# Performance work log

Measured on AMD Instinct MI355X. Metric: run time of the kernel, lower is better.

## Reference

```python
import jax, jax.numpy as jnp
import numpy as np

OUT_IMG = 256
OUT_MSK = 64


def _src_coords(n_out, size):
    # F.interpolate bilinear align_corners=False source coordinates, clamped to edge
    sizef = size.astype(jnp.float32)
    t = (jnp.arange(n_out, dtype=jnp.float32) + 0.5) * (sizef / n_out) - 0.5
    t = jnp.clip(t, 0.0, sizef - 1.0)
    t0 = jnp.floor(t).astype(jnp.int32)
    t1 = jnp.minimum(t0 + 1, size - 1)
    return t0, t1, t - t0.astype(jnp.float32)


def _per_sample(x_img, x_msk, x_bg, pad, sel, color):
    # x_img [3,H,W] float, x_msk [H,W] bool, x_bg [3,Hb,Wb], pad [4] int (l,r,t,b)
    H, W = x_msk.shape
    ys = jnp.any(x_msk, axis=1)
    xs = jnp.any(x_msk, axis=0)
    iy = jnp.arange(H)
    ix = jnp.arange(W)
    miny = jnp.min(jnp.where(ys, iy, H))
    maxy = jnp.max(jnp.where(ys, iy, -1))
    minx = jnp.min(jnp.where(xs, ix, W))
    maxx = jnp.max(jnp.where(xs, ix, -1))
    h = maxy - miny + 1
    w = maxx - minx + 1
    left, right, top, bot = pad[0], pad[1], pad[2], pad[3]
    Hp = h + top + bot   # padded crop height
    Wp = w + left + right  # padded crop width
    # background: real bg image or solid random color (c[ii][-1] > 2 branch)
    bg_sel = jnp.where(sel > 2, x_bg, jnp.broadcast_to(color[:, None, None], x_bg.shape))

    def mask_at(P, Q):
        # value of the padded-cropped mask at integer padded coords (P, Q)
        in_crop = (P >= top) & (P < top + h) & (Q >= left) & (Q < left + w)
        r = jnp.clip(miny + P - top, 0, H - 1)
        c = jnp.clip(minx + Q - left, 0, W - 1)
        return in_crop & x_msk[r, c], r, c

    def sample_img(py, px):
        # composited padded image at integer coords (py x px grid) -> [3,Ho,Wo]
        P = py[:, None]
        Q = px[None, :]
        m, r, c = mask_at(P, Q)
        iv = x_img[:, r, c]
        bv = bg_sel[:, P, Q]
        return jnp.where(m[None], iv, bv)

    def sample_msk(py, px):
        m, _, _ = mask_at(py[:, None], px[None, :])
        return m.astype(jnp.float32)

    def bilinear(sample_fn, n_out, ch_leading):
        y0, y1, wy = _src_coords(n_out, Hp)
        x0, x1, wx = _src_coords(n_out, Wp)
        s00 = sample_fn(y0, x0)
        s01 = sample_fn(y0, x1)
        s10 = sample_fn(y1, x0)
        s11 = sample_fn(y1, x1)
        wy_ = wy[:, None]
        wx_ = wx[None, :]
        if ch_leading:
            wy_ = wy_[None]
            wx_ = wx_[None]
        top_row = s00 * (1.0 - wx_) + s01 * wx_
        bot_row = s10 * (1.0 - wx_) + s11 * wx_
        return top_row * (1.0 - wy_) + bot_row * wy_

    img_out = bilinear(sample_img, OUT_IMG, True)        # [3,256,256]
    msk_out = bilinear(sample_msk, OUT_MSK, False)[None]  # [1,64,64]
    return img_out, msk_out


def _rgb_to_hsv(x):
    r, g, b = x[:, 0], x[:, 1], x[:, 2]
    mx = jnp.max(x, axis=1)
    mn = jnp.min(x, axis=1)
    d = mx - mn
    ds = jnp.where(d > 0, d, 1.0)
    hr = ((g - b) / ds) % 6.0
    hg = (b - r) / ds + 2.0
    hb = (r - g) / ds + 4.0
    hch = jnp.where(mx == r, hr, jnp.where(mx == g, hg, hb)) / 6.0
    hch = jnp.where(d > 0, hch, 0.0)
    s = jnp.where(mx > 0, d / jnp.where(mx > 0, mx, 1.0), 0.0)
    return hch, s, mx


def _hsv_to_rgb(hch, s, v):
    h6 = hch * 6.0
    i = jnp.floor(h6)
    f = h6 - i
    p = v * (1.0 - s)
    q = v * (1.0 - f * s)
    t = v * (1.0 - (1.0 - f) * s)
    im = i.astype(jnp.int32) % 6
    conds = [im == 0, im == 1, im == 2, im == 3, im == 4, im == 5]
    r = jnp.select(conds, [v, q, p, p, t, v])
    g = jnp.select(conds, [t, v, v, q, p, p])
    b = jnp.select(conds, [p, p, t, v, v, q])
    return jnp.stack([r, g, b], axis=1)


def _color_jitter(img, jit):
    # ColorJitter(0.1, 0.1, 0.1, 0.1) with explicit per-sample factors
    b = (0.9 + 0.2 * jit[:, 0])[:, None, None, None]
    c = (0.9 + 0.2 * jit[:, 1])[:, None, None, None]
    s = (0.9 + 0.2 * jit[:, 2])[:, None, None, None]
    hd = (-0.1 + 0.2 * jit[:, 3])[:, None, None]
    img = jnp.clip(img * b, 0.0, 1.0)
    gray = (0.299 * img[:, 0] + 0.587 * img[:, 1] + 0.114 * img[:, 2])[:, None]
    mean = jnp.mean(gray, axis=(2, 3), keepdims=True)
    img = jnp.clip(c * img + (1.0 - c) * mean, 0.0, 1.0)
    gray = (0.299 * img[:, 0] + 0.587 * img[:, 1] + 0.114 * img[:, 2])[:, None]
    img = jnp.clip(s * img + (1.0 - s) * gray, 0.0, 1.0)
    hch, sa, v = _rgb_to_hsv(img)
    hch = (hch + hd) % 1.0
    return jnp.clip(_hsv_to_rgb(hch, sa, v), 0.0, 1.0)


def setup_inputs() -> dict:
    key = jax.random.key(0)
    ks = jax.random.split(key, 7)
    B, H, W = 64, 448, 448
    return {
        "img": jax.random.uniform(ks[0], (B, 3, H, W), jnp.float32),
        "ms": jax.random.uniform(ks[1], (B, 1, H, W), jnp.float32),
        "bg": jax.random.uniform(ks[2], (B, 3, H + 40, W + 40), jnp.float32),
        "pads": jax.random.randint(ks[3], (B, 4), 0, 20, jnp.int32),
        "csel": jax.random.randint(ks[4], (B,), 0, 20, jnp.int32),
        "rand_color": jax.random.uniform(ks[5], (B, 3), jnp.float32),
        "jitter": jax.random.uniform(ks[6], (B, 4), jnp.float32),
    }


def reference(img, ms, bg, pads, csel, rand_color, jitter):
    mask = ms[:, 0] > 0.5
    img_out, msk_out = jax.vmap(_per_sample)(img, mask, bg, pads, csel, rand_color)
    img_out = _color_jitter(img_out, jitter)
    return img_out, msk_out
```

## Files before the change

kernel.cpp:

```cpp
#include <hip/hip_runtime.h>

#define H_IN 448
#define W_IN 448
#define HW_IN (H_IN * W_IN)
#define BGW 488
#define BGHW (BGW * BGW)
#define OUTI 256
#define OUTI_PIX (OUTI * OUTI)
#define OUTM 64
#define B_SAMPLES 64
#define BBOX_CHUNKS 16
#define BBOX_ROWS (H_IN / BBOX_CHUNKS)
#define BITS_STRIDE 8

typedef unsigned long long u64;

__device__ __forceinline__ float clamp01(float x) { return fminf(fmaxf(x, 0.f), 1.f); }
__device__ __forceinline__ int clampi(int x, int lo, int hi) { return min(max(x, lo), hi); }

__global__ void k_bbox(const float* __restrict__ ms, int* __restrict__ bbox,
                       u64* __restrict__ bits) {
    int b = blockIdx.y, chunk = blockIdx.x;
    int tid = threadIdx.x;
    int wave = tid >> 6, lane = tid & 63;
    const float* msB = ms + (size_t)b * HW_IN;
    u64* bitsB = bits + (size_t)b * H_IN * BITS_STRIDE;

    int miny = H_IN, maxy = -1, minx = W_IN, maxx = -1;
    for (int rr = wave; rr < BBOX_ROWS; rr += 4) {
        int row = chunk * BBOX_ROWS + rr;
        const float4* rowp = (const float4*)(msB + (size_t)row * W_IN);
#pragma unroll
        for (int sub = 0; sub < 2; ++sub) {
            int c4 = sub * 64 + lane;
            bool valid = c4 < (W_IN / 4);
            float4 v = rowp[min(c4, W_IN / 4 - 1)];
            bool a0 = valid && (v.x > 0.5f);
            bool a1 = valid && (v.y > 0.5f);
            bool a2 = valid && (v.z > 0.5f);
            bool a3 = valid && (v.w > 0.5f);
            u64 b0 = __ballot(a0), b1 = __ballot(a1), b2 = __ballot(a2), b3 = __ballot(a3);
            if (a0 | a1 | a2 | a3) {
                miny = min(miny, row); maxy = max(maxy, row);
                int xb = c4 * 4;
                if (a0) { minx = min(minx, xb);     maxx = max(maxx, xb); }
                if (a1) { minx = min(minx, xb + 1); maxx = max(maxx, xb + 1); }
                if (a2) { minx = min(minx, xb + 2); maxx = max(maxx, xb + 2); }
                if (a3) { minx = min(minx, xb + 3); maxx = max(maxx, xb + 3); }
            }
            if (lane < 4) {
                u64 w = (lane == 0) ? b0 : (lane == 1) ? b1 : (lane == 2) ? b2 : b3;
                bitsB[(size_t)row * BITS_STRIDE + sub * 4 + lane] = w;
            }
        }
    }
    __shared__ int s[4];
    if (tid == 0) { s[0] = H_IN; s[1] = -1; s[2] = W_IN; s[3] = -1; }
    __syncthreads();
    atomicMin(&s[0], miny); atomicMax(&s[1], maxy);
    atomicMin(&s[2], minx); atomicMax(&s[3], maxx);
    __syncthreads();
    if (tid == 0) {
        atomicMin(&bbox[b * 4 + 0], s[0]);
        atomicMin(&bbox[b * 4 + 1], -s[1]);
        atomicMin(&bbox[b * 4 + 2], s[2]);
        atomicMin(&bbox[b * 4 + 3], -s[3]);
    }
}

struct Geo {
    int miny, minx, h, w, top, left, Hp, Wp;
};
__device__ __forceinline__ Geo load_geo(const int* __restrict__ bbox,
                                        const int* __restrict__ pads, int b) {
    Geo g;
    g.miny = bbox[b * 4 + 0];
    int maxy = -bbox[b * 4 + 1];
    g.minx = bbox[b * 4 + 2];
    int maxx = -bbox[b * 4 + 3];
    int left = pads[b * 4 + 0], right = pads[b * 4 + 1];
    int top = pads[b * 4 + 2], bot = pads[b * 4 + 3];
    g.h = maxy - g.miny + 1;
    g.w = maxx - g.minx + 1;
    g.top = top; g.left = left;
    g.Hp = g.h + top + bot;
    g.Wp = g.w + left + right;
    return g;
}

__device__ __forceinline__ void src_coord(int i, int n_out, int size,
                                          int& t0, int& t1, float& frac) {
    float sizef = (float)size;
    float t = (i + 0.5f) * (sizef / (float)n_out) - 0.5f;
    t = fminf(fmaxf(t, 0.f), sizef - 1.f);
    t0 = (int)floorf(t);
    t1 = min(t0 + 1, size - 1);
    frac = t - (float)t0;
}

__device__ __forceinline__ bool mask_bit(const u64* rowbits, int c) {
    u64 w = rowbits[((c >> 8) << 2) | (c & 3)];
    return (w >> ((c >> 2) & 63)) & 1ULL;
}

__global__ void __launch_bounds__(256) k_resize_img(
        const float* __restrict__ img, const float* __restrict__ bg,
        const int* __restrict__ pads, const int* __restrict__ csel,
        const float* __restrict__ rcol, const float* __restrict__ jit,
        const int* __restrict__ bbox, const u64* __restrict__ bits,
        unsigned short* __restrict__ mid, float* __restrict__ partials) {
    int oy = blockIdx.x;
    int b = blockIdx.y;
    int tid = threadIdx.x;

    Geo g = load_geo(bbox, pads, b);
    bool useBg = csel[b] > 2;
    float c0 = rcol[b * 3 + 0], c1 = rcol[b * 3 + 1], c2 = rcol[b * 3 + 2];
    float bfac = 0.9f + 0.2f * jit[b * 4 + 0];

    int y0, y1; float wy;
    src_coord(oy, OUTI, g.Hp, y0, y1, wy);
    int r0 = clampi(g.miny + y0 - g.top, 0, H_IN - 1);
    int r1 = clampi(g.miny + y1 - g.top, 0, H_IN - 1);
    bool incy0 = (y0 >= g.top) && (y0 < g.top + g.h);
    bool incy1 = (y1 >= g.top) && (y1 < g.top + g.h);

    __shared__ float s_im[6][W_IN];
    __shared__ float s_bg[6][BGW];
    __shared__ u64 s_bits[2][BITS_STRIDE];

    const float* imB = img + (size_t)b * 3 * HW_IN;
    const u64* bitsB = bits + (size_t)b * H_IN * BITS_STRIDE;

#pragma unroll
    for (int k = 0; k < 3; ++k) {
        int item = k * 256 + tid;
        int p = item >> 7;
        int idx = item & 127;
        if (idx < W_IN / 4) {
            int ky = p > 2;
            int ch = p - 3 * ky;
            int row = ky ? r1 : r0;
            ((float4*)s_im[p])[idx] =
                ((const float4*)(imB + (size_t)ch * HW_IN + (size_t)row * W_IN))[idx];
        }
    }
    if (useBg) {
        const float* bgB = bg + (size_t)b * 3 * BGHW;
#pragma unroll
        for (int k = 0; k < 3; ++k) {
            int item = k * 256 + tid;
            int p = item >> 7;
            int idx = item & 127;
            if (idx < BGW / 4) {
                int ky = p > 2;
                int ch = p - 3 * ky;
                int row = ky ? y1 : y0;
                ((float4*)s_bg[p])[idx] =
                    ((const float4*)(bgB + (size_t)ch * BGHW + (size_t)row * BGW))[idx];
            }
        }
    }
    if (tid < 16) {
        int ky = tid >> 3, idx = tid & 7;
        s_bits[ky][idx] = bitsB[(size_t)(ky ? r1 : r0) * BITS_STRIDE + idx];
    }
    __syncthreads();

    int x0, x1; float wx;
    src_coord(tid, OUTI, g.Wp, x0, x1, wx);

    float acc0 = 0.f, acc1 = 0.f, acc2 = 0.f;
#pragma unroll
    for (int tap = 0; tap < 4; ++tap) {
        int ky = tap >> 1;
        int ky3 = ky * 3;
        int Q = (tap & 1) ? x1 : x0;
        float wgt = (ky ? wy : 1.f - wy) * ((tap & 1) ? wx : 1.f - wx);
        bool incy = ky ? incy1 : incy0;
        bool in_crop = incy && (Q >= g.left) && (Q < g.left + g.w);
        int c = clampi(g.minx + Q - g.left, 0, W_IN - 1);
        bool mm = in_crop && mask_bit(s_bits[ky], c);
        float i0 = s_im[ky3 + 0][c], i1 = s_im[ky3 + 1][c], i2 = s_im[ky3 + 2][c];
        float b0, b1, b2;
        if (useBg) {
            b0 = s_bg[ky3 + 0][Q]; b1 = s_bg[ky3 + 1][Q]; b2 = s_bg[ky3 + 2][Q];
        } else {
            b0 = c0; b1 = c1; b2 = c2;
        }
        acc0 += wgt * (mm ? i0 : b0);
        acc1 += wgt * (mm ? i1 : b1);
        acc2 += wgt * (mm ? i2 : b2);
    }
    float o0 = clamp01(acc0 * bfac);
    float o1 = clamp01(acc1 * bfac);
    float o2 = clamp01(acc2 * bfac);
    size_t o = (size_t)b * 3 * OUTI_PIX + (size_t)oy * OUTI + tid;
    mid[o] = (unsigned short)__float2uint_rn(o0 * 65535.f);
    mid[o + OUTI_PIX] = (unsigned short)__float2uint_rn(o1 * 65535.f);
    mid[o + 2 * OUTI_PIX] = (unsigned short)__float2uint_rn(o2 * 65535.f);

    float gsum = 0.299f * o0 + 0.587f * o1 + 0.114f * o2;
#pragma unroll
    for (int off = 32; off > 0; off >>= 1) gsum += __shfl_down(gsum, off, 64);
    __shared__ float ls[4];
    int wid = tid >> 6, lane = tid & 63;
    if (lane == 0) ls[wid] = gsum;
    __syncthreads();
    if (tid == 0)
        partials[b * 256 + oy] = ls[0] + ls[1] + ls[2] + ls[3];
}

__global__ void k_resize_msk(const u64* __restrict__ bits, const int* __restrict__ pads,
                             const int* __restrict__ bbox, float* __restrict__ outm) {
    int b = blockIdx.y;
    int pix = blockIdx.x * blockDim.x + threadIdx.x;
    int oy = pix >> 6, ox = pix & 63;

    Geo g = load_geo(bbox, pads, b);
    int y0, y1, x0, x1; float wy, wx;
    src_coord(oy, OUTM, g.Hp, y0, y1, wy);
    src_coord(ox, OUTM, g.Wp, x0, x1, wx);

    const u64* bitsB = bits + (size_t)b * H_IN * BITS_STRIDE;
    float acc = 0.f;
#pragma unroll
    for (int tap = 0; tap < 4; ++tap) {
        int P = (tap & 2) ? y1 : y0;
        int Q = (tap & 1) ? x1 : x0;
        float wgt = ((tap & 2) ? wy : 1.f - wy) * ((tap & 1) ? wx : 1.f - wx);
        bool in_crop = (P >= g.top) && (P < g.top + g.h) && (Q >= g.left) && (Q < g.left + g.w);
        int r = clampi(g.miny + P - g.top, 0, H_IN - 1);
        int c = clampi(g.minx + Q - g.left, 0, W_IN - 1);
        bool mm = in_crop && mask_bit(bitsB + (size_t)r * BITS_STRIDE, c);
        acc += wgt * (mm ? 1.f : 0.f);
    }
    outm[(size_t)b * (OUTM * OUTM) + pix] = acc;
}

__device__ __forceinline__ void jitter_px(float& r, float& g, float& bl,
                                          float cc, float ssf, float hd, float mean) {
    r = clamp01(cc * r + (1.f - cc) * mean);
    g = clamp01(cc * g + (1.f - cc) * mean);
    bl = clamp01(cc * bl + (1.f - cc) * mean);
    float gray = 0.299f * r + 0.587f * g + 0.114f * bl;
    r = clamp01(ssf * r + (1.f - ssf) * gray);
    g = clamp01(ssf * g + (1.f - ssf) * gray);
    bl = clamp01(ssf * bl + (1.f - ssf) * gray);
    float mx = fmaxf(r, fmaxf(g, bl));
    float mn = fminf(r, fminf(g, bl));
    float d = mx - mn;
    float dsv = (d > 0.f) ? d : 1.f;
    float hch;
    if (mx == r) {
        float t = (g - bl) / dsv;
        t = fmodf(t, 6.f);
        if (t < 0.f) t += 6.f;
        hch = t;
    } else if (mx == g) {
        hch = (bl - r) / dsv + 2.f;
    } else {
        hch = (r - g) / dsv + 4.f;
    }
    hch = (d > 0.f) ? hch * (1.f / 6.f) : 0.f;
    float sat = (mx > 0.f) ? d / mx : 0.f;
    float v = mx;
    float hh = hch + hd;
    hh -= floorf(hh);
    float h6 = hh * 6.f;
    float fi = floorf(h6);
    float f = h6 - fi;
    float pp = v * (1.f - sat);
    float q = v * (1.f - f * sat);
    float t = v * (1.f - (1.f - f) * sat);
    int im = ((int)fi) % 6;
    float ro, go, bo;
    switch (im) {
        case 0: ro = v;  go = t;  bo = pp; break;
        case 1: ro = q;  go = v;  bo = pp; break;
        case 2: ro = pp; go = v;  bo = t;  break;
        case 3: ro = pp; go = q;  bo = v;  break;
        case 4: ro = t;  go = pp; bo = v;  break;
        default: ro = v; go = pp; bo = q;  break;
    }
    r = clamp01(ro); g = clamp01(go); bl = clamp01(bo);
}

__global__ void k_jitter(const unsigned short* __restrict__ mid,
                         float* __restrict__ out, const float* __restrict__ jit,
                         const float* __restrict__ partials) {
    int b = blockIdx.y;
    int tid = threadIdx.x;

    float pv = partials[b * 256 + tid];
#pragma unroll
    for (int off = 32; off > 0; off >>= 1) pv += __shfl_down(pv, off, 64);
    __shared__ float ls[4];
    int wid = tid >> 6, lane = tid & 63;
    if (lane == 0) ls[wid] = pv;
    __syncthreads();
    float mean = (ls[0] + ls[1] + ls[2] + ls[3]) * (1.f / (float)OUTI_PIX);

    float cc = 0.9f + 0.2f * jit[b * 4 + 1];
    float ssf = 0.9f + 0.2f * jit[b * 4 + 2];
    float hd = -0.1f + 0.2f * jit[b * 4 + 3];

    int idx4 = blockIdx.x * blockDim.x + tid;
    const ushort4* mr = (const ushort4*)(mid + (size_t)b * 3 * OUTI_PIX) + idx4;
    const ushort4* mg = mr + OUTI_PIX / 4;
    const ushort4* mb = mr + 2 * (OUTI_PIX / 4);
    ushort4 ur = *mr, ug = *mg, ub = *mb;

    const float S = 1.f / 65535.f;
    float r0 = ur.x * S, r1 = ur.y * S, r2 = ur.z * S, r3 = ur.w * S;
    float g0 = ug.x * S, g1 = ug.y * S, g2 = ug.z * S, g3 = ug.w * S;
    float b0 = ub.x * S, b1 = ub.y * S, b2 = ub.z * S, b3 = ub.w * S;

    jitter_px(r0, g0, b0, cc, ssf, hd, mean);
    jitter_px(r1, g1, b1, cc, ssf, hd, mean);
    jitter_px(r2, g2, b2, cc, ssf, hd, mean);
    jitter_px(r3, g3, b3, cc, ssf, hd, mean);

    float4* pr = (float4*)(out + (size_t)b * 3 * OUTI_PIX) + idx4;
    float4* pg = pr + OUTI_PIX / 4;
    float4* pb = pr + 2 * (OUTI_PIX / 4);
    *pr = make_float4(r0, r1, r2, r3);
    *pg = make_float4(g0, g1, g2, g3);
    *pb = make_float4(b0, b1, b2, b3);
}

extern "C" void kernel_launch(void* const* d_in, const int* in_sizes, int n_in,
                              void* d_out, int out_size, void* d_ws, size_t ws_size,
                              hipStream_t stream) {
    const float* img = (const float*)d_in[0];
    const float* ms = (const float*)d_in[1];
    const float* bg = (const float*)d_in[2];
    const int* pads = (const int*)d_in[3];
    const int* csel = (const int*)d_in[4];
    const float* rcol = (const float*)d_in[5];
    const float* jit = (const float*)d_in[6];
    float* out = (float*)d_out;

    int* bbox = (int*)d_ws;
    float* partials = (float*)((char*)d_ws + 1024);
    u64* bits = (u64*)((char*)d_ws + 1024 + 65536);
    unsigned short* mid = (unsigned short*)((char*)d_ws + (2u << 20));
    float* outm = out + (size_t)B_SAMPLES * 3 * OUTI_PIX;

    hipMemsetAsync(bbox, 0x7F, B_SAMPLES * 4 * sizeof(int), stream);

    k_bbox<<<dim3(BBOX_CHUNKS, B_SAMPLES), 256, 0, stream>>>(ms, bbox, bits);
    k_resize_img<<<dim3(OUTI, B_SAMPLES), 256, 0, stream>>>(
        img, bg, pads, csel, rcol, jit, bbox, bits, mid, partials);
    k_resize_msk<<<dim3((OUTM * OUTM) / 256, B_SAMPLES), 256, 0, stream>>>(
        bits, pads, bbox, outm);
    k_jitter<<<dim3(OUTI_PIX / 4 / 256, B_SAMPLES), 256, 0, stream>>>(
        mid, out, jit, partials);
}
```

Before: 123.3 us.

## Process four output rows per block, sharing a u16-quantized source row span

Each resize block now computes four consecutive output rows. It loads the contiguous span of image and background source rows once into shared memory, stored as 16-bit values. This cuts the repeated global loads of overlapping source rows and quarters the block count, with the per-row gray partial sums folded into one value per group. The cost is that inputs are quantized to 16 bits before interpolation, which adds a small precision loss, and the shared-memory span is fixed at ten rows.

```diff
diff --git a/kernel.cpp b/kernel.cpp
--- a/kernel.cpp
+++ b/kernel.cpp
@@ -12,6 +12,9 @@
 #define BBOX_CHUNKS 16
 #define BBOX_ROWS (H_IN / BBOX_CHUNKS)
 #define BITS_STRIDE 8
+#define RPB 4
+#define NGRP (OUTI / RPB)
+#define SPAN 10
 
 typedef unsigned long long u64;
 
@@ -103,13 +106,32 @@
     return (w >> ((c >> 2) & 63)) & 1ULL;
 }
 
+struct RowGeom {
+    int y0, y1, r0, r1;
+    float wy;
+    bool incy0, incy1;
+};
+__device__ __forceinline__ RowGeom row_geom(const Geo& g, int oy) {
+    RowGeom rg;
+    src_coord(oy, OUTI, g.Hp, rg.y0, rg.y1, rg.wy);
+    rg.r0 = clampi(g.miny + rg.y0 - g.top, 0, H_IN - 1);
+    rg.r1 = clampi(g.miny + rg.y1 - g.top, 0, H_IN - 1);
+    rg.incy0 = (rg.y0 >= g.top) && (rg.y0 < g.top + g.h);
+    rg.incy1 = (rg.y1 >= g.top) && (rg.y1 < g.top + g.h);
+    return rg;
+}
+
+__device__ __forceinline__ unsigned short q16(float x) {
+    return (unsigned short)__float2uint_rn(x * 65535.f);
+}
+
 __global__ void __launch_bounds__(256) k_resize_img(
         const float* __restrict__ img, const float* __restrict__ bg,
         const int* __restrict__ pads, const int* __restrict__ csel,
         const float* __restrict__ rcol, const float* __restrict__ jit,
         const int* __restrict__ bbox, const u64* __restrict__ bits,
         unsigned short* __restrict__ mid, float* __restrict__ partials) {
-    int oy = blockIdx.x;
+    int grp = blockIdx.x;
     int b = blockIdx.y;
     int tid = threadIdx.x;
 
@@ -118,97 +140,110 @@
     float c0 = rcol[b * 3 + 0], c1 = rcol[b * 3 + 1], c2 = rcol[b * 3 + 2];
     float bfac = 0.9f + 0.2f * jit[b * 4 + 0];
 
-    int y0, y1; float wy;
-    src_coord(oy, OUTI, g.Hp, y0, y1, wy);
-    int r0 = clampi(g.miny + y0 - g.top, 0, H_IN - 1);
-    int r1 = clampi(g.miny + y1 - g.top, 0, H_IN - 1);
-    bool incy0 = (y0 >= g.top) && (y0 < g.top + g.h);
-    bool incy1 = (y1 >= g.top) && (y1 < g.top + g.h);
-
-    __shared__ float s_im[6][W_IN];
-    __shared__ float s_bg[6][BGW];
-    __shared__ u64 s_bits[2][BITS_STRIDE];
+    RowGeom rg[RPB];
+#pragma unroll
+    for (int t = 0; t < RPB; ++t) rg[t] = row_geom(g, grp * RPB + t);
+    int R0 = rg[0].r0, R1 = rg[RPB - 1].r1;
+    int Y0 = rg[0].y0, Y1 = rg[RPB - 1].y1;
+    int NRi = R1 - R0 + 1;
+    int NRb = Y1 - Y0 + 1;
+
+    __shared__ unsigned short s_im[3][SPAN][W_IN];
+    __shared__ unsigned short s_bg[3][SPAN][BGW];
+    __shared__ u64 s_bits[SPAN][BITS_STRIDE];
+    __shared__ float ls[4];
 
     const float* imB = img + (size_t)b * 3 * HW_IN;
     const u64* bitsB = bits + (size_t)b * H_IN * BITS_STRIDE;
 
 #pragma unroll
-    for (int k = 0; k < 3; ++k) {
-        int item = k * 256 + tid;
-        int p = item >> 7;
-        int idx = item & 127;
-        if (idx < W_IN / 4) {
-            int ky = p > 2;
-            int ch = p - 3 * ky;
-            int row = ky ? r1 : r0;
-            ((float4*)s_im[p])[idx] =
-                ((const float4*)(imB + (size_t)ch * HW_IN + (size_t)row * W_IN))[idx];
+    for (int ch = 0; ch < 3; ++ch) {
+        const float4* src = (const float4*)(imB + (size_t)ch * HW_IN + (size_t)R0 * W_IN);
+        int n4 = NRi * (W_IN / 4);
+        for (int i = tid; i < n4; i += 256) {
+            int row = i / (W_IN / 4);
+            int idx = i - row * (W_IN / 4);
+            float4 v = src[i];
+            ushort4 u = {q16(v.x), q16(v.y), q16(v.z), q16(v.w)};
+            *(ushort4*)&s_im[ch][row][idx * 4] = u;
         }
     }
     if (useBg) {
         const float* bgB = bg + (size_t)b * 3 * BGHW;
 #pragma unroll
-        for (int k = 0; k < 3; ++k) {
-            int item = k * 256 + tid;
-            int p = item >> 7;
-            int idx = item & 127;
-            if (idx < BGW / 4) {
-                int ky = p > 2;
-                int ch = p - 3 * ky;
-                int row = ky ? y1 : y0;
-                ((float4*)s_bg[p])[idx] =
-                    ((const float4*)(bgB + (size_t)ch * BGHW + (size_t)row * BGW))[idx];
+        for (int ch = 0; ch < 3; ++ch) {
+            const float4* src = (const float4*)(bgB + (size_t)ch * BGHW + (size_t)Y0 * BGW);
+            int n4 = NRb * (BGW / 4);
+            for (int i = tid; i < n4; i += 256) {
+                int row = i / (BGW / 4);
+                int idx = i - row * (BGW / 4);
+                float4 v = src[i];
+                ushort4 u = {q16(v.x), q16(v.y), q16(v.z), q16(v.w)};
+                *(ushort4*)&s_bg[ch][row][idx * 4] = u;
             }
         }
     }
-    if (tid < 16) {
-        int ky = tid >> 3, idx = tid & 7;
-        s_bits[ky][idx] = bitsB[(size_t)(ky ? r1 : r0) * BITS_STRIDE + idx];
+    if (tid < NRi * BITS_STRIDE) {
+        int row = tid >> 3, idx = tid & 7;
+        s_bits[row][idx] = bitsB[(size_t)(R0 + row) * BITS_STRIDE + idx];
     }
     __syncthreads();
 
     int x0, x1; float wx;
     src_coord(tid, OUTI, g.Wp, x0, x1, wx);
-
-    float acc0 = 0.f, acc1 = 0.f, acc2 = 0.f;
-#pragma unroll
-    for (int tap = 0; tap < 4; ++tap) {
-        int ky = tap >> 1;
-        int ky3 = ky * 3;
-        int Q = (tap & 1) ? x1 : x0;
-        float wgt = (ky ? wy : 1.f - wy) * ((tap & 1) ? wx : 1.f - wx);
-        bool incy = ky ? incy1 : incy0;
-        bool in_crop = incy && (Q >= g.left) && (Q < g.left + g.w);
-        int c = clampi(g.minx + Q - g.left, 0, W_IN - 1);
-        bool mm = in_crop && mask_bit(s_bits[ky], c);
-        float i0 = s_im[ky3 + 0][c], i1 = s_im[ky3 + 1][c], i2 = s_im[ky3 + 2][c];
-        float b0, b1, b2;
-        if (useBg) {
-            b0 = s_bg[ky3 + 0][Q]; b1 = s_bg[ky3 + 1][Q]; b2 = s_bg[ky3 + 2][Q];
-        } else {
-            b0 = c0; b1 = c1; b2 = c2;
+    int cA = clampi(g.minx + x0 - g.left, 0, W_IN - 1);
+    int cB = clampi(g.minx + x1 - g.left, 0, W_IN - 1);
+    bool inxA = (x0 >= g.left) && (x0 < g.left + g.w);
+    bool inxB = (x1 >= g.left) && (x1 < g.left + g.w);
+
+    const float S = 1.f / 65535.f;
+    float gacc = 0.f;
+#pragma unroll
+    for (int t = 0; t < RPB; ++t) {
+        float acc0 = 0.f, acc1 = 0.f, acc2 = 0.f;
+#pragma unroll
+        for (int tap = 0; tap < 4; ++tap) {
+            int ky = tap >> 1;
+            int Q = (tap & 1) ? x1 : x0;
+            int c = (tap & 1) ? cB : cA;
+            float wgt = (ky ? rg[t].wy : 1.f - rg[t].wy) * ((tap & 1) ? wx : 1.f - wx);
+            bool incy = ky ? rg[t].incy1 : rg[t].incy0;
+            bool in_crop = incy && ((tap & 1) ? inxB : inxA);
+            int rr = (ky ? rg[t].r1 : rg[t].r0) - R0;
+            bool mm = in_crop && mask_bit(s_bits[rr], c);
+            float i0 = s_im[0][rr][c] * S;
+            float i1 = s_im[1][rr][c] * S;
+            float i2 = s_im[2][rr][c] * S;
+            float b0, b1, b2;
+            if (useBg) {
+                int br = (ky ? rg[t].y1 : rg[t].y0) - Y0;
+                b0 = s_bg[0][br][Q] * S;
+                b1 = s_bg[1][br][Q] * S;
+                b2 = s_bg[2][br][Q] * S;
+            } else {
+                b0 = c0; b1 = c1; b2 = c2;
+            }
+            acc0 += wgt * (mm ? i0 : b0);
+            acc1 += wgt * (mm ? i1 : b1);
+            acc2 += wgt * (mm ? i2 : b2);
         }
-        acc0 += wgt * (mm ? i0 : b0);
-        acc1 += wgt * (mm ? i1 : b1);
-        acc2 += wgt * (mm ? i2 : b2);
-    }
-    float o0 = clamp01(acc0 * bfac);
-    float o1 = clamp01(acc1 * bfac);
-    float o2 = clamp01(acc2 * bfac);
-    size_t o = (size_t)b * 3 * OUTI_PIX + (size_t)oy * OUTI + tid;
-    mid[o] = (unsigned short)__float2uint_rn(o0 * 65535.f);
-    mid[o + OUTI_PIX] = (unsigned short)__float2uint_rn(o1 * 65535.f);
-    mid[o + 2 * OUTI_PIX] = (unsigned short)__float2uint_rn(o2 * 65535.f);
-
-    float gsum = 0.299f * o0 + 0.587f * o1 + 0.114f * o2;
-#pragma unroll
-    for (int off = 32; off > 0; off >>= 1) gsum += __shfl_down(gsum, off, 64);
-    __shared__ float ls[4];
-    int wid = tid >> 6, lane = tid & 63;
-    if (lane == 0) ls[wid] = gsum;
+        float o0 = clamp01(acc0 * bfac);
+        float o1 = clamp01(acc1 * bfac);
+        float o2 = clamp01(acc2 * bfac);
+        size_t o = (size_t)b * 3 * OUTI_PIX + (size_t)(grp * RPB + t) * OUTI + tid;
+        mid[o] = q16(o0);
+        mid[o + OUTI_PIX] = q16(o1);
+        mid[o + 2 * OUTI_PIX] = q16(o2);
+        gacc += 0.299f * o0 + 0.587f * o1 + 0.114f * o2;
+    }
+
+#pragma unroll
+    for (int off = 32; off > 0; off >>= 1) gacc += __shfl_down(gacc, off, 64);
+    int wave = tid >> 6, lane = tid & 63;
+    if (lane == 0) ls[wave] = gacc;
     __syncthreads();
     if (tid == 0)
-        partials[b * 256 + oy] = ls[0] + ls[1] + ls[2] + ls[3];
+        partials[b * NGRP + grp] = ls[0] + ls[1] + ls[2] + ls[3];
 }
 
 __global__ void k_resize_msk(const u64* __restrict__ bits, const int* __restrict__ pads,
@@ -292,7 +327,7 @@
     int b = blockIdx.y;
     int tid = threadIdx.x;
 
-    float pv = partials[b * 256 + tid];
+    float pv = (tid < NGRP) ? partials[b * NGRP + tid] : 0.f;
 #pragma unroll
     for (int off = 32; off > 0; off >>= 1) pv += __shfl_down(pv, off, 64);
     __shared__ float ls[4];
@@ -350,7 +385,7 @@
     hipMemsetAsync(bbox, 0x7F, B_SAMPLES * 4 * sizeof(int), stream);
 
     k_bbox<<<dim3(BBOX_CHUNKS, B_SAMPLES), 256, 0, stream>>>(ms, bbox, bits);
-    k_resize_img<<<dim3(OUTI, B_SAMPLES), 256, 0, stream>>>(
+    k_resize_img<<<dim3(NGRP, B_SAMPLES), 256, 0, stream>>>(
         img, bg, pads, csel, rcol, jit, bbox, bits, mid, partials);
     k_resize_msk<<<dim3((OUTM * OUTM) / 256, B_SAMPLES), 256, 0, stream>>>(
         bits, pads, bbox, outm);
```

Measured after the change: 200.1 us. 62.3% more time.

## Split image resize rows into half-width blocks loading only a 256-column window

Applied to the files above, without the earlier changes.

Each output row of the image resize is now handled by two 128-thread blocks, each staging only a 256-column window of the source image and background rows into shared memory instead of the full rows. The point is to cut global loads and shared-memory footprint per block and to launch more, smaller blocks. Per-block brightness partials double and the jitter kernel sums both halves. The bbox kernel also gets twice as many chunks. The window assumes the source span of 128 output columns fits in 256 columns, which holds only when the padded crop width is at most about 512.

```diff
diff --git a/kernel.cpp b/kernel.cpp
--- a/kernel.cpp
+++ b/kernel.cpp
@@ -9,9 +9,10 @@
 #define OUTI_PIX (OUTI * OUTI)
 #define OUTM 64
 #define B_SAMPLES 64
-#define BBOX_CHUNKS 16
+#define BBOX_CHUNKS 32
 #define BBOX_ROWS (H_IN / BBOX_CHUNKS)
 #define BITS_STRIDE 8
+#define WIN 256
 
 typedef unsigned long long u64;
 
@@ -103,15 +104,22 @@
     return (w >> ((c >> 2) & 63)) & 1ULL;
 }
 
-__global__ void __launch_bounds__(256) k_resize_img(
+__device__ __forceinline__ unsigned short q16(float x) {
+    return (unsigned short)__float2uint_rn(x * 65535.f);
+}
+
+__global__ void __launch_bounds__(128) k_resize_img(
         const float* __restrict__ img, const float* __restrict__ bg,
         const int* __restrict__ pads, const int* __restrict__ csel,
         const float* __restrict__ rcol, const float* __restrict__ jit,
         const int* __restrict__ bbox, const u64* __restrict__ bits,
         unsigned short* __restrict__ mid, float* __restrict__ partials) {
-    int oy = blockIdx.x;
+    int bx = blockIdx.x;
+    int oy = bx >> 1;
+    int h = bx & 1;
     int b = blockIdx.y;
     int tid = threadIdx.x;
+    int col = h * 128 + tid;
 
     Geo g = load_geo(bbox, pads, b);
     bool useBg = csel[b] > 2;
@@ -125,40 +133,43 @@
     bool incy0 = (y0 >= g.top) && (y0 < g.top + g.h);
     bool incy1 = (y1 >= g.top) && (y1 < g.top + g.h);
 
-    __shared__ float s_im[6][W_IN];
-    __shared__ float s_bg[6][BGW];
+    int xw0, xw1d; float wdum;
+    src_coord(h * 128, OUTI, g.Wp, xw0, xw1d, wdum);
+    int cW = clampi(g.minx + xw0 - g.left, 0, W_IN - 1);
+    int cStart = min(cW & ~3, W_IN - WIN);
+    int qStart = min(xw0 & ~3, BGW - WIN);
+
+    __shared__ float s_im[6][WIN];
+    __shared__ float s_bg[6][WIN];
     __shared__ u64 s_bits[2][BITS_STRIDE];
+    __shared__ float ls[2];
 
     const float* imB = img + (size_t)b * 3 * HW_IN;
     const u64* bitsB = bits + (size_t)b * H_IN * BITS_STRIDE;
 
 #pragma unroll
     for (int k = 0; k < 3; ++k) {
-        int item = k * 256 + tid;
-        int p = item >> 7;
-        int idx = item & 127;
-        if (idx < W_IN / 4) {
+        int item = k * 128 + tid;
+        int p = item >> 6;
+        int idx = item & 63;
+        int ky = p > 2;
+        int ch = p - 3 * ky;
+        int row = ky ? r1 : r0;
+        ((float4*)s_im[p])[idx] =
+            ((const float4*)(imB + (size_t)ch * HW_IN + (size_t)row * W_IN + cStart))[idx];
+    }
+    if (useBg) {
+        const float* bgB = bg + (size_t)b * 3 * BGHW;
+#pragma unroll
+        for (int k = 0; k < 3; ++k) {
+            int item = k * 128 + tid;
+            int p = item >> 6;
+            int idx = item & 63;
             int ky = p > 2;
             int ch = p - 3 * ky;
-            int row = ky ? r1 : r0;
-            ((float4*)s_im[p])[idx] =
-                ((const float4*)(imB + (size_t)ch * HW_IN + (size_t)row * W_IN))[idx];
-        }
-    }
-    if (useBg) {
-        const float* bgB = bg + (size_t)b * 3 * BGHW;
-#pragma unroll
-        for (int k = 0; k < 3; ++k) {
-            int item = k * 256 + tid;
-            int p = item >> 7;
-            int idx = item & 127;
-            if (idx < BGW / 4) {
-                int ky = p > 2;
-                int ch = p - 3 * ky;
-                int row = ky ? y1 : y0;
-                ((float4*)s_bg[p])[idx] =
-                    ((const float4*)(bgB + (size_t)ch * BGHW + (size_t)row * BGW))[idx];
-            }
+            int row = ky ? y1 : y0;
+            ((float4*)s_bg[p])[idx] =
+                ((const float4*)(bgB + (size_t)ch * BGHW + (size_t)row * BGW + qStart))[idx];
         }
     }
     if (tid < 16) {
@@ -168,7 +179,7 @@
     __syncthreads();
 
     int x0, x1; float wx;
-    src_coord(tid, OUTI, g.Wp, x0, x1, wx);
+    src_coord(col, OUTI, g.Wp, x0, x1, wx);
 
     float acc0 = 0.f, acc1 = 0.f, acc2 = 0.f;
 #pragma unroll
@@ -181,10 +192,12 @@
         bool in_crop = incy && (Q >= g.left) && (Q < g.left + g.w);
         int c = clampi(g.minx + Q - g.left, 0, W_IN - 1);
         bool mm = in_crop && mask_bit(s_bits[ky], c);
-        float i0 = s_im[ky3 + 0][c], i1 = s_im[ky3 + 1][c], i2 = s_im[ky3 + 2][c];
+        int cl = c - cStart;
+        float i0 = s_im[ky3 + 0][cl], i1 = s_im[ky3 + 1][cl], i2 = s_im[ky3 + 2][cl];
         float b0, b1, b2;
         if (useBg) {
-            b0 = s_bg[ky3 + 0][Q]; b1 = s_bg[ky3 + 1][Q]; b2 = s_bg[ky3 + 2][Q];
+            int ql = Q - qStart;
+            b0 = s_bg[ky3 + 0][ql]; b1 = s_bg[ky3 + 1][ql]; b2 = s_bg[ky3 + 2][ql];
         } else {
             b0 = c0; b1 = c1; b2 = c2;
         }
@@ -195,20 +208,19 @@
     float o0 = clamp01(acc0 * bfac);
     float o1 = clamp01(acc1 * bfac);
     float o2 = clamp01(acc2 * bfac);
-    size_t o = (size_t)b * 3 * OUTI_PIX + (size_t)oy * OUTI + tid;
-    mid[o] = (unsigned short)__float2uint_rn(o0 * 65535.f);
-    mid[o + OUTI_PIX] = (unsigned short)__float2uint_rn(o1 * 65535.f);
-    mid[o + 2 * OUTI_PIX] = (unsigned short)__float2uint_rn(o2 * 65535.f);
+    size_t o = (size_t)b * 3 * OUTI_PIX + (size_t)oy * OUTI + col;
+    mid[o] = q16(o0);
+    mid[o + OUTI_PIX] = q16(o1);
+    mid[o + 2 * OUTI_PIX] = q16(o2);
 
     float gsum = 0.299f * o0 + 0.587f * o1 + 0.114f * o2;
 #pragma unroll
     for (int off = 32; off > 0; off >>= 1) gsum += __shfl_down(gsum, off, 64);
-    __shared__ float ls[4];
-    int wid = tid >> 6, lane = tid & 63;
-    if (lane == 0) ls[wid] = gsum;
+    int wave = tid >> 6, lane = tid & 63;
+    if (lane == 0) ls[wave] = gsum;
     __syncthreads();
     if (tid == 0)
-        partials[b * 256 + oy] = ls[0] + ls[1] + ls[2] + ls[3];
+        partials[b * 512 + bx] = ls[0] + ls[1];
 }
 
 __global__ void k_resize_msk(const u64* __restrict__ bits, const int* __restrict__ pads,
@@ -292,7 +304,7 @@
     int b = blockIdx.y;
     int tid = threadIdx.x;
 
-    float pv = partials[b * 256 + tid];
+    float pv = partials[b * 512 + tid] + partials[b * 512 + 256 + tid];
 #pragma unroll
     for (int off = 32; off > 0; off >>= 1) pv += __shfl_down(pv, off, 64);
     __shared__ float ls[4];
@@ -343,14 +355,14 @@
 
     int* bbox = (int*)d_ws;
     float* partials = (float*)((char*)d_ws + 1024);
-    u64* bits = (u64*)((char*)d_ws + 1024 + 65536);
+    u64* bits = (u64*)((char*)d_ws + 1024 + 512 * B_SAMPLES * 4);
     unsigned short* mid = (unsigned short*)((char*)d_ws + (2u << 20));
     float* outm = out + (size_t)B_SAMPLES * 3 * OUTI_PIX;
 
     hipMemsetAsync(bbox, 0x7F, B_SAMPLES * 4 * sizeof(int), stream);
 
     k_bbox<<<dim3(BBOX_CHUNKS, B_SAMPLES), 256, 0, stream>>>(ms, bbox, bits);
-    k_resize_img<<<dim3(OUTI, B_SAMPLES), 256, 0, stream>>>(
+    k_resize_img<<<dim3(OUTI * 2, B_SAMPLES), 128, 0, stream>>>(
         img, bg, pads, csel, rcol, jit, bbox, bits, mid, partials);
     k_resize_msk<<<dim3((OUTM * OUTM) / 256, B_SAMPLES), 256, 0, stream>>>(
         bits, pads, bbox, outm);
```

After: 137.2 us. +11.3%, slower.

## Process two output rows per block and stage source rows in LDS as 16-bit

Applied to the files above, without the earlier changes.

The image resize kernel now handles two output rows per 512-thread block instead of one row per 256-thread block, loading four source rows per block. The staged image and background rows are quantized to 16-bit unsigned in shared memory to halve LDS footprint and allow higher occupancy. Partial sums are reduced per row pair, and the jitter kernel is adjusted to read 128 partials. Adjacent output rows often share source rows, yet each row's pair is still loaded separately, so little global traffic is saved. The extra quantization adds conversion work and slight precision loss.

```diff
diff --git a/kernel.cpp b/kernel.cpp
--- a/kernel.cpp
+++ b/kernel.cpp
@@ -17,6 +17,9 @@
 
 __device__ __forceinline__ float clamp01(float x) { return fminf(fmaxf(x, 0.f), 1.f); }
 __device__ __forceinline__ int clampi(int x, int lo, int hi) { return min(max(x, lo), hi); }
+__device__ __forceinline__ unsigned short q16(float x) {
+    return (unsigned short)__float2uint_rn(x * 65535.f);
+}
 
 __global__ void k_bbox(const float* __restrict__ ms, int* __restrict__ bbox,
                        u64* __restrict__ bits) {
@@ -103,88 +106,114 @@
     return (w >> ((c >> 2) & 63)) & 1ULL;
 }
 
-__global__ void __launch_bounds__(256) k_resize_img(
+struct RowGeom {
+    int y0, y1, r0, r1;
+    float wy;
+    bool incy0, incy1;
+};
+__device__ __forceinline__ RowGeom row_geom(const Geo& g, int oy) {
+    RowGeom rg;
+    src_coord(oy, OUTI, g.Hp, rg.y0, rg.y1, rg.wy);
+    rg.r0 = clampi(g.miny + rg.y0 - g.top, 0, H_IN - 1);
+    rg.r1 = clampi(g.miny + rg.y1 - g.top, 0, H_IN - 1);
+    rg.incy0 = (rg.y0 >= g.top) && (rg.y0 < g.top + g.h);
+    rg.incy1 = (rg.y1 >= g.top) && (rg.y1 < g.top + g.h);
+    return rg;
+}
+
+__global__ void __launch_bounds__(512, 8) k_resize_img(
         const float* __restrict__ img, const float* __restrict__ bg,
         const int* __restrict__ pads, const int* __restrict__ csel,
         const float* __restrict__ rcol, const float* __restrict__ jit,
         const int* __restrict__ bbox, const u64* __restrict__ bits,
         unsigned short* __restrict__ mid, float* __restrict__ partials) {
-    int oy = blockIdx.x;
+    int pair = blockIdx.x;
     int b = blockIdx.y;
     int tid = threadIdx.x;
+    int trow = tid >> 8;
+    int col = tid & 255;
 
     Geo g = load_geo(bbox, pads, b);
     bool useBg = csel[b] > 2;
     float c0 = rcol[b * 3 + 0], c1 = rcol[b * 3 + 1], c2 = rcol[b * 3 + 2];
     float bfac = 0.9f + 0.2f * jit[b * 4 + 0];
 
-    int y0, y1; float wy;
-    src_coord(oy, OUTI, g.Hp, y0, y1, wy);
-    int r0 = clampi(g.miny + y0 - g.top, 0, H_IN - 1);
-    int r1 = clampi(g.miny + y1 - g.top, 0, H_IN - 1);
-    bool incy0 = (y0 >= g.top) && (y0 < g.top + g.h);
-    bool incy1 = (y1 >= g.top) && (y1 < g.top + g.h);
-
-    __shared__ float s_im[6][W_IN];
-    __shared__ float s_bg[6][BGW];
-    __shared__ u64 s_bits[2][BITS_STRIDE];
+    RowGeom rg0 = row_geom(g, pair * 2 + 0);
+    RowGeom rg1 = row_geom(g, pair * 2 + 1);
+
+    __shared__ unsigned short s_im[12][W_IN];
+    __shared__ unsigned short s_bg[12][BGW];
+    __shared__ u64 s_bits[4][BITS_STRIDE];
+    __shared__ float ls[8];
 
     const float* imB = img + (size_t)b * 3 * HW_IN;
     const u64* bitsB = bits + (size_t)b * H_IN * BITS_STRIDE;
 
 #pragma unroll
     for (int k = 0; k < 3; ++k) {
-        int item = k * 256 + tid;
+        int item = k * 512 + tid;
         int p = item >> 7;
         int idx = item & 127;
         if (idx < W_IN / 4) {
-            int ky = p > 2;
-            int ch = p - 3 * ky;
-            int row = ky ? r1 : r0;
-            ((float4*)s_im[p])[idx] =
-                ((const float4*)(imB + (size_t)ch * HW_IN + (size_t)row * W_IN))[idx];
+            int s = p / 3, ch = p - 3 * (p / 3);
+            int row = (s == 0) ? rg0.r0 : (s == 1) ? rg0.r1 : (s == 2) ? rg1.r0 : rg1.r1;
+            float4 v = ((const float4*)(imB + (size_t)ch * HW_IN + (size_t)row * W_IN))[idx];
+            ushort4 u = {q16(v.x), q16(v.y), q16(v.z), q16(v.w)};
+            *(ushort4*)&s_im[p][idx * 4] = u;
         }
     }
     if (useBg) {
         const float* bgB = bg + (size_t)b * 3 * BGHW;
 #pragma unroll
         for (int k = 0; k < 3; ++k) {
-            int item = k * 256 + tid;
+            int item = k * 512 + tid;
             int p = item >> 7;
             int idx = item & 127;
             if (idx < BGW / 4) {
-                int ky = p > 2;
-                int ch = p - 3 * ky;
-                int row = ky ? y1 : y0;
-                ((float4*)s_bg[p])[idx] =
-                    ((const float4*)(bgB + (size_t)ch * BGHW + (size_t)row * BGW))[idx];
+                int s = p / 3, ch = p - 3 * (p / 3);
+                int row = (s == 0) ? rg0.y0 : (s == 1) ? rg0.y1 : (s == 2) ? rg1.y0 : rg1.y1;
+                float4 v = ((const float4*)(bgB + (size_t)ch * BGHW + (size_t)row * BGW))[idx];
+                ushort4 u = {q16(v.x), q16(v.y), q16(v.z), q16(v.w)};
+                *(ushort4*)&s_bg[p][idx * 4] = u;
             }
         }
     }
-    if (tid < 16) {
-        int ky = tid >> 3, idx = tid & 7;
-        s_bits[ky][idx] = bitsB[(size_t)(ky ? r1 : r0) * BITS_STRIDE + idx];
-    }
-    __syncthreads();
+    if (tid < 32) {
+        int s = tid >> 3, idx = tid & 7;
+        int row = (s == 0) ? rg0.r0 : (s == 1) ? rg0.r1 : (s == 2) ? rg1.r0 : rg1.r1;
+        s_bits[s][idx] = bitsB[(size_t)row * BITS_STRIDE + idx];
+    }
+    __syncthreads();
+
+    RowGeom rgt;
+    rgt.wy = trow ? rg1.wy : rg0.wy;
+    rgt.incy0 = trow ? rg1.incy0 : rg0.incy0;
+    rgt.incy1 = trow ? rg1.incy1 : rg0.incy1;
 
     int x0, x1; float wx;
-    src_coord(tid, OUTI, g.Wp, x0, x1, wx);
-
+    src_coord(col, OUTI, g.Wp, x0, x1, wx);
+
+    const float S = 1.f / 65535.f;
     float acc0 = 0.f, acc1 = 0.f, acc2 = 0.f;
 #pragma unroll
     for (int tap = 0; tap < 4; ++tap) {
         int ky = tap >> 1;
-        int ky3 = ky * 3;
+        int slot = trow * 2 + ky;
+        int p3 = slot * 3;
         int Q = (tap & 1) ? x1 : x0;
-        float wgt = (ky ? wy : 1.f - wy) * ((tap & 1) ? wx : 1.f - wx);
-        bool incy = ky ? incy1 : incy0;
+        float wgt = (ky ? rgt.wy : 1.f - rgt.wy) * ((tap & 1) ? wx : 1.f - wx);
+        bool incy = ky ? rgt.incy1 : rgt.incy0;
         bool in_crop = incy && (Q >= g.left) && (Q < g.left + g.w);
         int c = clampi(g.minx + Q - g.left, 0, W_IN - 1);
-        bool mm = in_crop && mask_bit(s_bits[ky], c);
-        float i0 = s_im[ky3 + 0][c], i1 = s_im[ky3 + 1][c], i2 = s_im[ky3 + 2][c];
+        bool mm = in_crop && mask_bit(s_bits[slot], c);
+        float i0 = s_im[p3 + 0][c] * S;
+        float i1 = s_im[p3 + 1][c] * S;
+        float i2 = s_im[p3 + 2][c] * S;
         float b0, b1, b2;
         if (useBg) {
-            b0 = s_bg[ky3 + 0][Q]; b1 = s_bg[ky3 + 1][Q]; b2 = s_bg[ky3 + 2][Q];
+            b0 = s_bg[p3 + 0][Q] * S;
+            b1 = s_bg[p3 + 1][Q] * S;
+            b2 = s_bg[p3 + 2][Q] * S;
         } else {
             b0 = c0; b1 = c1; b2 = c2;
         }
@@ -195,20 +224,24 @@
     float o0 = clamp01(acc0 * bfac);
     float o1 = clamp01(acc1 * bfac);
     float o2 = clamp01(acc2 * bfac);
-    size_t o = (size_t)b * 3 * OUTI_PIX + (size_t)oy * OUTI + tid;
-    mid[o] = (unsigned short)__float2uint_rn(o0 * 65535.f);
-    mid[o + OUTI_PIX] = (unsigned short)__float2uint_rn(o1 * 65535.f);
-    mid[o + 2 * OUTI_PIX] = (unsigned short)__float2uint_rn(o2 * 65535.f);
+    int oy = pair * 2 + trow;
+    size_t o = (size_t)b * 3 * OUTI_PIX + (size_t)oy * OUTI + col;
+    mid[o] = q16(o0);
+    mid[o + OUTI_PIX] = q16(o1);
+    mid[o + 2 * OUTI_PIX] = q16(o2);
 
     float gsum = 0.299f * o0 + 0.587f * o1 + 0.114f * o2;
 #pragma unroll
     for (int off = 32; off > 0; off >>= 1) gsum += __shfl_down(gsum, off, 64);
-    __shared__ float ls[4];
-    int wid = tid >> 6, lane = tid & 63;
-    if (lane == 0) ls[wid] = gsum;
-    __syncthreads();
-    if (tid == 0)
-        partials[b * 256 + oy] = ls[0] + ls[1] + ls[2] + ls[3];
+    int wave = tid >> 6, lane = tid & 63;
+    if (lane == 0) ls[wave] = gsum;
+    __syncthreads();
+    if (tid == 0) {
+        float t = 0.f;
+#pragma unroll
+        for (int k = 0; k < 8; ++k) t += ls[k];
+        partials[b * 128 + pair] = t;
+    }
 }
 
 __global__ void k_resize_msk(const u64* __restrict__ bits, const int* __restrict__ pads,
@@ -292,7 +325,7 @@
     int b = blockIdx.y;
     int tid = threadIdx.x;
 
-    float pv = partials[b * 256 + tid];
+    float pv = (tid < 128) ? partials[b * 128 + tid] : 0.f;
 #pragma unroll
     for (int off = 32; off > 0; off >>= 1) pv += __shfl_down(pv, off, 64);
     __shared__ float ls[4];
@@ -350,7 +383,7 @@
     hipMemsetAsync(bbox, 0x7F, B_SAMPLES * 4 * sizeof(int), stream);
 
     k_bbox<<<dim3(BBOX_CHUNKS, B_SAMPLES), 256, 0, stream>>>(ms, bbox, bits);
-    k_resize_img<<<dim3(OUTI, B_SAMPLES), 256, 0, stream>>>(
+    k_resize_img<<<dim3(OUTI / 2, B_SAMPLES), 512, 0, stream>>>(
         img, bg, pads, csel, rcol, jit, bbox, bits, mid, partials);
     k_resize_msk<<<dim3((OUTM * OUTM) / 256, B_SAMPLES), 256, 0, stream>>>(
         bits, pads, bbox, outm);
```

After: 125.1 us. Within noise of the previous version (+1.5%).
